# Optimization experiments

Measured on AMD Instinct MI355X. Metric: run time of the kernel, lower is better.

Reference implementation:

```python
import jax, jax.numpy as jnp
import numpy as np

H, DH = 16, 64          # num_heads, dim_head
DIM = 1024              # dim_ltn
EPS = 1e-5


def setup_inputs() -> dict:
    key = jax.random.key(0)
    ks = jax.random.split(key, 8)
    b, n_txt, t, m = 2, 2048, 4, 256
    text = jax.random.normal(ks[0], (b, n_txt, DIM), dtype=jnp.float32)
    image = jax.random.normal(ks[1], (b, t, m, DIM), dtype=jnp.float32)
    locations = jax.random.randint(ks[2], (b, n_txt), 0, 2)  # 0/1 media markers
    s = DIM ** -0.5
    Wq = jax.random.normal(ks[3], (DIM, H * DH), dtype=jnp.float32) * s
    Wkv = jax.random.normal(ks[4], (DIM, 2 * H * DH), dtype=jnp.float32) * s
    Wo = jax.random.normal(ks[5], (H * DH, DIM), dtype=jnp.float32) * s
    ln_gamma = jnp.ones((DIM,), dtype=jnp.float32)
    ln_beta = jnp.zeros((DIM,), dtype=jnp.float32)
    return {"text": text, "image": image, "locations": locations,
            "Wq": Wq, "Wkv": Wkv, "Wo": Wo,
            "ln_gamma": ln_gamma, "ln_beta": ln_beta}


def reference(text, image, locations, Wq, Wkv, Wo, ln_gamma, ln_beta):
    scale = DH ** -0.5
    b, t, m, d = image.shape
    # LayerNorm(text)
    mu = text.mean(-1, keepdims=True)
    var = ((text - mu) ** 2).mean(-1, keepdims=True)
    tn = (text - mu) / jnp.sqrt(var + EPS) * ln_gamma + ln_beta
    img = image.reshape(b, t * m, d)             # b (t m) d
    q = tn @ Wq                                  # b n (h dh)
    k, v = jnp.split(img @ Wkv, 2, axis=-1)      # each b tm (h dh)
    split_heads = lambda x: x.reshape(x.shape[0], x.shape[1], H, DH).transpose(0, 2, 1, 3)
    q, k, v = split_heads(q), split_heads(k), split_heads(v)
    attn = jnp.einsum('bhid,bhjd->bhij', q, k) * scale   # b h n (t m)
    txt_time = jnp.cumsum(locations, axis=-1)            # b n : media index per text token
    viz_time = jnp.repeat(jnp.arange(1, t + 1), m)       # (t m)
    # only_attend_to_immediate -> equality mask
    mask = txt_time[:, None, :, None] == viz_time[None, None, None, :]
    neg = -jnp.finfo(attn.dtype).max
    attn = jnp.where(mask, attn, neg)
    attn = jax.nn.softmax(attn, axis=-1)
    # zero attention for text tokens before any media (txt_time == 0)
    attn = jnp.where((txt_time == 0)[:, None, :, None], 0.0, attn)
    out = jnp.einsum('bhij,bhjd->bhid', attn, v)
    out = out.transpose(0, 2, 1, 3).reshape(b, -1, H * DH)
    return out @ Wo
```

## Files before the change

kernel.cpp:

```cpp
#include <hip/hip_runtime.h>

#define BATCH 2
#define NTXT  2048
#define TMED  4
#define MMED  256
#define TM    (TMED * MMED)
#define DIM   1024
#define NH    16
#define DHD   64
#define KVW   2048
#define RMAX  256
#define RT    32

typedef _Float16 f16x8 __attribute__((ext_vector_type(8)));
typedef float    f32x4 __attribute__((ext_vector_type(4)));

__global__ __launch_bounds__(1024) void k1_scan_ibar(
    const int* __restrict__ loc, const float* __restrict__ image,
    int* __restrict__ tt, int* __restrict__ seg, float* __restrict__ ibar,
    _Float16* __restrict__ img16) {
  __shared__ int buf[NTXT];
  __shared__ int s_start, s_end;
  const int idx = blockIdx.x;
  const int tid = threadIdx.x;
  if (idx < BATCH) {
    const int b = idx;
    if (tid == 0) { s_start = NTXT; s_end = NTXT; }
    buf[tid]        = loc[b * NTXT + tid];
    buf[tid + 1024] = loc[b * NTXT + tid + 1024];
    __syncthreads();
    for (int off = 1; off < NTXT; off <<= 1) {
      int a0 = (tid >= off) ? buf[tid - off] : 0;
      int a1 = buf[tid + 1024 - off];
      __syncthreads();
      buf[tid] += a0;
      buf[tid + 1024] += a1;
      __syncthreads();
    }
    const int v0 = buf[tid], v1 = buf[tid + 1024];
    tt[b * NTXT + tid]        = v0;
    tt[b * NTXT + tid + 1024] = v1;
    if (v0 >= 1) atomicMin(&s_start, tid);
    if (v0 >= 5) atomicMin(&s_end, tid);
    if (v1 >= 1) atomicMin(&s_start, tid + 1024);
    if (v1 >= 5) atomicMin(&s_end, tid + 1024);
    __syncthreads();
    if (tid == 0) {
      seg[b * 2]     = s_start;
      seg[b * 2 + 1] = s_end - s_start;
    }
  } else {
    const int j = idx - BATCH;
    const int b = j >> 3, rt = j & 7;
    const size_t base = (size_t)(b * TM + rt * 128) * DIM + tid;
    const float* p = image + base;
    _Float16* q = img16 + base;
    float s = 0.f;
#pragma unroll 4
    for (int r = 0; r < 128; r++) {
      const float v = p[(size_t)r * DIM];
      s += v;
      q[(size_t)r * DIM] = (_Float16)v;
    }
    atomicAdd(&ibar[b * DIM + tid], s * (1.0f / (float)TM));
  }
}

__global__ __launch_bounds__(256) void k2_prep(
    const float* __restrict__ Wkv, const float* __restrict__ text,
    const float* __restrict__ gamma, const float* __restrict__ beta,
    const int* __restrict__ seg, const float* __restrict__ ibar,
    _Float16* __restrict__ WkvT, float* __restrict__ tn,
    float* __restrict__ vbar) {
  __shared__ float tile[64][65];
  __shared__ float red[256];
  const int idx = blockIdx.x;
  const int tid = threadIdx.x;
  if (idx < 512) {
    const int k0 = (idx & 15) * 64, n0 = (idx >> 4) * 64;
    const int r = tid >> 4, c4 = (tid & 15) * 4;
#pragma unroll
    for (int i = 0; i < 4; i++) {
      const float4 v = *reinterpret_cast<const float4*>(
          Wkv + (size_t)(k0 + r + i * 16) * KVW + n0 + c4);
      tile[r + i * 16][c4 + 0] = v.x; tile[r + i * 16][c4 + 1] = v.y;
      tile[r + i * 16][c4 + 2] = v.z; tile[r + i * 16][c4 + 3] = v.w;
    }
    __syncthreads();
#pragma unroll
    for (int it = 0; it < 2; it++) {
      const int chunk = it * 256 + tid;
      const int n = chunk >> 3, kc = (chunk & 7) * 8;
      f16x8 h;
#pragma unroll
      for (int j = 0; j < 8; j++) h[j] = (_Float16)tile[kc + j][n];
      *reinterpret_cast<f16x8*>(WkvT + (size_t)(n0 + n) * DIM + k0 + kc) = h;
    }
  } else if (idx < 576) {
    const int j = idx - 512;
    const int b = j >> 5, rt = j & 31;
    const int i0 = seg[b * 2];
    const int cnt = min(seg[b * 2 + 1], RMAX);
    for (int r = rt; r < cnt; r += RT) {
      const float* xrow = text + (size_t)(b * NTXT + i0 + r) * DIM;
      float x[4];
      float s = 0.f;
#pragma unroll
      for (int u = 0; u < 4; u++) { x[u] = xrow[tid + 256 * u]; s += x[u]; }
      red[tid] = s; __syncthreads();
      for (int st = 128; st > 0; st >>= 1) {
        if (tid < st) red[tid] += red[tid + st];
        __syncthreads();
      }
      const float mu = red[0] * (1.0f / DIM); __syncthreads();
      float vs = 0.f;
#pragma unroll
      for (int u = 0; u < 4; u++) { float d = x[u] - mu; vs += d * d; }
      red[tid] = vs; __syncthreads();
      for (int st = 128; st > 0; st >>= 1) {
        if (tid < st) red[tid] += red[tid + st];
        __syncthreads();
      }
      const float rstd = rsqrtf(red[0] * (1.0f / DIM) + 1e-5f); __syncthreads();
      float* trow = tn + (size_t)(b * RMAX + r) * DIM;
#pragma unroll
      for (int u = 0; u < 4; u++) {
        const int c = tid + 256 * u;
        trow[c] = (x[u] - mu) * rstd * gamma[c] + beta[c];
      }
      __syncthreads();
    }
  } else {
    const int j = idx - 576;
    const int b = j >> 5, et = (j >> 3) & 3, cc = j & 7;
    const int e = et * 256 + tid;
    const int c0 = cc * 128;
    if (tid < 128) red[tid] = ibar[b * DIM + c0 + tid];
    __syncthreads();
    float s = 0.f;
    for (int c = 0; c < 128; c++)
      s += red[c] * Wkv[(size_t)(c0 + c) * KVW + DIM + e];
    atomicAdd(&vbar[b * DIM + e], s);
  }
}

__global__ __launch_bounds__(512) void k3_gemm_qproj_obar(
    const _Float16* __restrict__ img16, const _Float16* __restrict__ WkvT,
    const float* __restrict__ Wq, const float* __restrict__ Wo,
    const float* __restrict__ tn, const float* __restrict__ vbar,
    const int* __restrict__ seg, _Float16* __restrict__ kv16,
    float* __restrict__ qbuf, float* __restrict__ obar) {
  __shared__ char smem[16384];
  const int idx = blockIdx.x;
  const int tid = threadIdx.x;
  if (idx < 256) {
    _Float16* As = (_Float16*)smem;
    _Float16* Bs = As + 128 * 32;
    const int lane = tid & 63, wid = tid >> 6;
    const int wm = wid & 3, wn = wid >> 2;
    const int row0 = (idx >> 4) * 128, col0 = (idx & 15) * 128;
    const int srow = tid >> 2, skc = (tid & 3) * 8;
    const int frow = lane & 15, fq = lane >> 4;
    f32x4 acc[2][4] = {};
    for (int k0 = 0; k0 < DIM; k0 += 32) {
      const f16x8 av = *reinterpret_cast<const f16x8*>(
          img16 + (size_t)(row0 + srow) * DIM + k0 + skc);
      const f16x8 bv = *reinterpret_cast<const f16x8*>(
          WkvT + (size_t)(col0 + srow) * DIM + k0 + skc);
      __syncthreads();
      *reinterpret_cast<f16x8*>(As + tid * 8) = av;
      *reinterpret_cast<f16x8*>(Bs + tid * 8) = bv;
      __syncthreads();
      f16x8 af[2], bf[4];
#pragma unroll
      for (int mt = 0; mt < 2; mt++)
        af[mt] = *reinterpret_cast<const f16x8*>(
            As + (wm * 32 + mt * 16 + frow) * 32 + fq * 8);
#pragma unroll
      for (int nt = 0; nt < 4; nt++)
        bf[nt] = *reinterpret_cast<const f16x8*>(
            Bs + (wn * 64 + nt * 16 + frow) * 32 + fq * 8);
#pragma unroll
      for (int mt = 0; mt < 2; mt++)
#pragma unroll
        for (int nt = 0; nt < 4; nt++)
          acc[mt][nt] = __builtin_amdgcn_mfma_f32_16x16x32_f16(
              af[mt], bf[nt], acc[mt][nt], 0, 0, 0);
    }
#pragma unroll
    for (int mt = 0; mt < 2; mt++)
#pragma unroll
      for (int nt = 0; nt < 4; nt++) {
        const int col = col0 + wn * 64 + nt * 16 + frow;
#pragma unroll
        for (int r = 0; r < 4; r++) {
          const int row = row0 + wm * 32 + mt * 16 + fq * 4 + r;
          kv16[(size_t)row * KVW + col] = (_Float16)acc[mt][nt][r];
        }
      }
  } else if (idx < 320) {
    float* tn_s = (float*)smem;
    const int j = idx - 256;
    const int b = j >> 5, nt = (j >> 2) & 7, cc = j & 3;
    const int n0 = nt * 128, c0 = cc * 256;
    const int n = tid & 127, cs = tid >> 7;
    const int cnt = min(seg[b * 2 + 1], RMAX);
    for (int r0 = 0; r0 < cnt; r0 += 8) {
      const int rows = min(8, cnt - r0);
      for (int i = tid; i < 8 * 256; i += 512) {
        const int r = i >> 8, c = i & 255;
        tn_s[i] = (r < rows) ? tn[(size_t)(b * RMAX + r0 + r) * DIM + c0 + c]
                             : 0.f;
      }
      __syncthreads();
      float acc[8] = {};
      for (int ci = 0; ci < 64; ci++) {
        const int c = cs * 64 + ci;
        const float w = Wq[(size_t)(c0 + c) * DIM + n0 + n];
#pragma unroll
        for (int rr = 0; rr < 8; rr++) acc[rr] += tn_s[rr * 256 + c] * w;
      }
      for (int rr = 0; rr < rows; rr++)
        atomicAdd(&qbuf[(size_t)(b * RMAX + r0 + rr) * DIM + n0 + n], acc[rr]);
      __syncthreads();
    }
  } else {
    float* vb_s = (float*)smem;
    const int j = idx - 320;
    const int b = j >> 4, et = (j >> 3) & 1, cc = j & 7;
    const int e = et * 512 + tid;
    const int c0 = cc * 128;
    if (tid < 128) vb_s[tid] = vbar[b * DIM + c0 + tid];
    __syncthreads();
    float s = 0.f;
    for (int c = 0; c < 128; c++)
      s += vb_s[c] * Wo[(size_t)(c0 + c) * DIM + e];
    atomicAdd(&obar[b * DIM + e], s);
  }
}

__global__ __launch_bounds__(256) void k4_fill_attn(
    const float* __restrict__ text, const _Float16* __restrict__ kv16,
    const float* __restrict__ Wq, const float* __restrict__ Wo,
    const float* __restrict__ gamma, const float* __restrict__ beta,
    const int* __restrict__ tt, const int* __restrict__ seg,
    const float* __restrict__ obar, const float* __restrict__ qbuf,
    float* __restrict__ oacc, float* __restrict__ out) {
  __shared__ float red[256];
  __shared__ float pbuf[256];
  const int idx = blockIdx.x;
  const int tid = threadIdx.x;
  if (idx < BATCH * NTXT) {
    const int b = idx >> 11;
    const int i = idx & (NTXT - 1);
    const int t = tt[b * NTXT + i];
    float* orow = out + (size_t)(b * NTXT + i) * DIM;
    if (t == 0) {
      for (int c = tid; c < DIM; c += 256) orow[c] = 0.f;
      return;
    }
    if (t > TMED) {
      const float* ob = obar + b * DIM;
      for (int c = tid; c < DIM; c += 256) orow[c] = ob[c];
      return;
    }
    if (i - seg[b * 2] < RMAX) return;
    __shared__ float tns[DIM];
    __shared__ float qrow[DIM];
    __shared__ float oaccs[DIM];
    const float* xrow = text + (size_t)(b * NTXT + i) * DIM;
    float x[4];
    float s = 0.f;
#pragma unroll
    for (int u = 0; u < 4; u++) { x[u] = xrow[tid + 256 * u]; s += x[u]; }
    red[tid] = s; __syncthreads();
    for (int st = 128; st > 0; st >>= 1) {
      if (tid < st) red[tid] += red[tid + st];
      __syncthreads();
    }
    const float mu = red[0] * (1.0f / DIM); __syncthreads();
    float vs = 0.f;
#pragma unroll
    for (int u = 0; u < 4; u++) { float d = x[u] - mu; vs += d * d; }
    red[tid] = vs; __syncthreads();
    for (int st = 128; st > 0; st >>= 1) {
      if (tid < st) red[tid] += red[tid + st];
      __syncthreads();
    }
    const float rstd = rsqrtf(red[0] * (1.0f / DIM) + 1e-5f); __syncthreads();
#pragma unroll
    for (int u = 0; u < 4; u++) {
      const int c = tid + 256 * u;
      tns[c] = (x[u] - mu) * rstd * gamma[c] + beta[c];
    }
    __syncthreads();
    {
      float qa[4] = {0.f, 0.f, 0.f, 0.f};
      for (int c = 0; c < DIM; c++) {
        const float tv = tns[c];
        const float* w = Wq + (size_t)c * DIM + tid;
#pragma unroll
        for (int u = 0; u < 4; u++) qa[u] += tv * w[256 * u];
      }
#pragma unroll
      for (int u = 0; u < 4; u++) qrow[tid + 256 * u] = qa[u];
    }
    __syncthreads();
    const size_t kvrow0 = (size_t)(b * TM + (t - 1) * MMED) * KVW;
    const int d0 = tid & 63, g = tid >> 6;
    for (int h = 0; h < NH; h++) {
      const _Float16* krow = kv16 + kvrow0 + (size_t)tid * KVW + h * DHD;
      float sc = 0.f;
#pragma unroll
      for (int d = 0; d < DHD; d++) sc += qrow[h * DHD + d] * (float)krow[d];
      sc *= 0.125f;
      red[tid] = sc; __syncthreads();
      for (int st = 128; st > 0; st >>= 1) {
        if (tid < st) red[tid] = fmaxf(red[tid], red[tid + st]);
        __syncthreads();
      }
      const float mx = red[0]; __syncthreads();
      const float e = __expf(sc - mx);
      red[tid] = e; __syncthreads();
      for (int st = 128; st > 0; st >>= 1) {
        if (tid < st) red[tid] += red[tid + st];
        __syncthreads();
      }
      const float inv = 1.0f / red[0]; __syncthreads();
      pbuf[tid] = e * inv; __syncthreads();
      const _Float16* vbase = kv16 + kvrow0 + (size_t)(g * 64) * KVW + DIM + h * DHD + d0;
      float a = 0.f;
#pragma unroll 8
      for (int jj = 0; jj < 64; jj++) a += pbuf[g * 64 + jj] * (float)vbase[(size_t)jj * KVW];
      red[tid] = a; __syncthreads();
      if (tid < 64)
        oaccs[h * DHD + tid] = red[tid] + red[64 + tid] + red[128 + tid] + red[192 + tid];
      __syncthreads();
    }
    float oa[4] = {0.f, 0.f, 0.f, 0.f};
    for (int c = 0; c < DIM; c++) {
      const float ov = oaccs[c];
      const float* w = Wo + (size_t)c * DIM + tid;
#pragma unroll
      for (int u = 0; u < 4; u++) oa[u] += ov * w[256 * u];
    }
#pragma unroll
    for (int u = 0; u < 4; u++) orow[tid + 256 * u] = oa[u];
  } else {
    __shared__ float qs[DHD];
    const int j = idx - BATCH * NTXT;
    const int h = j & 15, rt = (j >> 4) & 31, b = j >> 9;
    const int i0 = seg[b * 2];
    const int cnt = min(seg[b * 2 + 1], RMAX);
    const int d0 = tid & 63, g = tid >> 6;
    for (int r = rt; r < cnt; r += RT) {
      const int i = i0 + r;
      const int t = tt[b * NTXT + i];
      if (tid < 64) qs[tid] = qbuf[(size_t)(b * RMAX + r) * DIM + h * DHD + tid];
      __syncthreads();
      const size_t kvrow0 = (size_t)(b * TM + (t - 1) * MMED) * KVW;
      const _Float16* krow = kv16 + kvrow0 + (size_t)tid * KVW + h * DHD;
      float sc = 0.f;
#pragma unroll
      for (int d = 0; d < DHD; d += 8) {
        const f16x8 kk = *reinterpret_cast<const f16x8*>(krow + d);
#pragma unroll
        for (int u = 0; u < 8; u++) sc += qs[d + u] * (float)kk[u];
      }
      sc *= 0.125f;
      red[tid] = sc; __syncthreads();
      for (int st = 128; st > 0; st >>= 1) {
        if (tid < st) red[tid] = fmaxf(red[tid], red[tid + st]);
        __syncthreads();
      }
      const float mx = red[0]; __syncthreads();
      const float e = __expf(sc - mx);
      red[tid] = e; __syncthreads();
      for (int st = 128; st > 0; st >>= 1) {
        if (tid < st) red[tid] += red[tid + st];
        __syncthreads();
      }
      const float inv = 1.0f / red[0]; __syncthreads();
      pbuf[tid] = e * inv; __syncthreads();
      const _Float16* vbase = kv16 + kvrow0 + (size_t)(g * 64) * KVW + DIM + h * DHD + d0;
      float a = 0.f;
#pragma unroll 8
      for (int jj = 0; jj < 64; jj++) a += pbuf[g * 64 + jj] * (float)vbase[(size_t)jj * KVW];
      red[tid] = a; __syncthreads();
      if (tid < 64)
        oacc[(size_t)(b * RMAX + r) * DIM + h * DHD + tid] =
            red[tid] + red[64 + tid] + red[128 + tid] + red[192 + tid];
      __syncthreads();
    }
  }
}

__global__ __launch_bounds__(256) void k5_oproj(
    const float* __restrict__ oacc, const float* __restrict__ Wo,
    const int* __restrict__ seg, float* __restrict__ out) {
  const int ct = blockIdx.x;
  const int rt = blockIdx.y;
  const int b = blockIdx.z;
  const int i0 = seg[b * 2];
  const int cnt = min(seg[b * 2 + 1], RMAX);
  const int tid = threadIdx.x;
  const int d0 = tid & 63, g = tid >> 6;
  __shared__ float op[4][64];
  for (int r = rt; r < cnt; r += RT) {
    const float* arow = oacc + (size_t)(b * RMAX + r) * DIM;
    const float* wo = Wo + (size_t)(g * 256) * DIM + ct * 64 + d0;
    float s = 0.f;
    for (int c = 0; c < 256; c++) s += arow[g * 256 + c] * wo[(size_t)c * DIM];
    op[g][d0] = s; __syncthreads();
    if (tid < 64)
      out[(size_t)(b * NTXT + i0 + r) * DIM + ct * 64 + tid] =
          op[0][tid] + op[1][tid] + op[2][tid] + op[3][tid];
    __syncthreads();
  }
}

extern "C" void kernel_launch(void* const* d_in, const int* in_sizes, int n_in,
                              void* d_out, int out_size, void* d_ws, size_t ws_size,
                              hipStream_t stream) {
  const float* text  = (const float*)d_in[0];
  const float* image = (const float*)d_in[1];
  const int*   loc   = (const int*)d_in[2];
  const float* Wq    = (const float*)d_in[3];
  const float* Wkv   = (const float*)d_in[4];
  const float* Wo    = (const float*)d_in[5];
  const float* gamma = (const float*)d_in[6];
  const float* beta  = (const float*)d_in[7];
  float* out = (float*)d_out;

  _Float16* kv16  = (_Float16*)d_ws;
  _Float16* WkvT  = kv16 + (size_t)BATCH * TM * KVW;
  float*    oacc  = (float*)WkvT;
  _Float16* img16 = WkvT + (size_t)KVW * DIM;
  float*    tn    = (float*)(img16 + (size_t)BATCH * TM * DIM);
  float*    qbuf  = tn + (size_t)BATCH * RMAX * DIM;
  float*    ibar  = qbuf + (size_t)BATCH * RMAX * DIM;
  float*    vbar  = ibar + BATCH * DIM;
  float*    obar  = vbar + BATCH * DIM;
  int*      tt    = (int*)(obar + BATCH * DIM);
  int*      seg   = tt + BATCH * NTXT;

  hipMemsetAsync(qbuf, 0,
                 ((size_t)BATCH * RMAX * DIM + 3 * BATCH * DIM) * sizeof(float),
                 stream);
  k1_scan_ibar<<<BATCH + 16, 1024, 0, stream>>>(loc, image, tt, seg, ibar, img16);
  k2_prep<<<640, 256, 0, stream>>>(Wkv, text, gamma, beta, seg, ibar,
                                   WkvT, tn, vbar);
  k3_gemm_qproj_obar<<<352, 512, 0, stream>>>(img16, WkvT, Wq, Wo, tn, vbar,
                                              seg, kv16, qbuf, obar);
  k4_fill_attn<<<BATCH * NTXT + NH * RT * BATCH, 256, 0, stream>>>(
      text, kv16, Wq, Wo, gamma, beta, tt, seg, obar, qbuf, oacc, out);
  k5_oproj<<<dim3(16, RT, BATCH), 256, 0, stream>>>(oacc, Wo, seg, out);
}
```

Before: 159.3 us.

## Fuse image fp16 conversion into KV GEMM and replace q atomics with partial buffers

The separate fp32-to-fp16 copy of the image in the scan kernel is removed. The KV GEMM now loads fp32 image rows directly and converts them in registers, which saves a full write and re-read of the half-precision image. The image-mean reduction is spread across 128 blocks instead of 16 to raise parallelism. The Q projection reduces its four column-slice partials in shared memory and writes them to four separate partial buffers, which the attention kernel sums when loading q, so the atomics and the large memset go away. The cost is that the GEMM reads twice as many bytes for its A operand.

```diff
diff --git a/kernel.cpp b/kernel.cpp
--- a/kernel.cpp
+++ b/kernel.cpp
@@ -11,14 +11,14 @@
 #define KVW   2048
 #define RMAX  256
 #define RT    32
+#define QSTR  ((size_t)BATCH * RMAX * DIM)
 
 typedef _Float16 f16x8 __attribute__((ext_vector_type(8)));
 typedef float    f32x4 __attribute__((ext_vector_type(4)));
 
 __global__ __launch_bounds__(1024) void k1_scan_ibar(
     const int* __restrict__ loc, const float* __restrict__ image,
-    int* __restrict__ tt, int* __restrict__ seg, float* __restrict__ ibar,
-    _Float16* __restrict__ img16) {
+    int* __restrict__ tt, int* __restrict__ seg, float* __restrict__ ibar) {
   __shared__ int buf[NTXT];
   __shared__ int s_start, s_end;
   const int idx = blockIdx.x;
@@ -51,17 +51,11 @@
     }
   } else {
     const int j = idx - BATCH;
-    const int b = j >> 3, rt = j & 7;
-    const size_t base = (size_t)(b * TM + rt * 128) * DIM + tid;
-    const float* p = image + base;
-    _Float16* q = img16 + base;
+    const int b = j >> 6, rt = j & 63;
+    const float* p = image + (size_t)(b * TM + rt * 16) * DIM + tid;
     float s = 0.f;
-#pragma unroll 4
-    for (int r = 0; r < 128; r++) {
-      const float v = p[(size_t)r * DIM];
-      s += v;
-      q[(size_t)r * DIM] = (_Float16)v;
-    }
+#pragma unroll
+    for (int r = 0; r < 16; r++) s += p[(size_t)r * DIM];
     atomicAdd(&ibar[b * DIM + tid], s * (1.0f / (float)TM));
   }
 }
@@ -145,12 +139,12 @@
 }
 
 __global__ __launch_bounds__(512) void k3_gemm_qproj_obar(
-    const _Float16* __restrict__ img16, const _Float16* __restrict__ WkvT,
+    const float* __restrict__ image, const _Float16* __restrict__ WkvT,
     const float* __restrict__ Wq, const float* __restrict__ Wo,
     const float* __restrict__ tn, const float* __restrict__ vbar,
     const int* __restrict__ seg, _Float16* __restrict__ kv16,
-    float* __restrict__ qbuf, float* __restrict__ obar) {
-  __shared__ char smem[16384];
+    float* __restrict__ qpart, float* __restrict__ obar) {
+  __shared__ char smem[24576];
   const int idx = blockIdx.x;
   const int tid = threadIdx.x;
   if (idx < 256) {
@@ -163,8 +157,14 @@
     const int frow = lane & 15, fq = lane >> 4;
     f32x4 acc[2][4] = {};
     for (int k0 = 0; k0 < DIM; k0 += 32) {
-      const f16x8 av = *reinterpret_cast<const f16x8*>(
-          img16 + (size_t)(row0 + srow) * DIM + k0 + skc);
+      const float* ap = image + (size_t)(row0 + srow) * DIM + k0 + skc;
+      const float4 a0 = *reinterpret_cast<const float4*>(ap);
+      const float4 a1 = *reinterpret_cast<const float4*>(ap + 4);
+      f16x8 av;
+      av[0] = (_Float16)a0.x; av[1] = (_Float16)a0.y;
+      av[2] = (_Float16)a0.z; av[3] = (_Float16)a0.w;
+      av[4] = (_Float16)a1.x; av[5] = (_Float16)a1.y;
+      av[6] = (_Float16)a1.z; av[7] = (_Float16)a1.w;
       const f16x8 bv = *reinterpret_cast<const f16x8*>(
           WkvT + (size_t)(col0 + srow) * DIM + k0 + skc);
       __syncthreads();
@@ -200,11 +200,13 @@
       }
   } else if (idx < 320) {
     float* tn_s = (float*)smem;
+    float* qred = tn_s + 8 * 256;
     const int j = idx - 256;
     const int b = j >> 5, nt = (j >> 2) & 7, cc = j & 3;
     const int n0 = nt * 128, c0 = cc * 256;
     const int n = tid & 127, cs = tid >> 7;
     const int cnt = min(seg[b * 2 + 1], RMAX);
+    float* qp = qpart + (size_t)cc * QSTR;
     for (int r0 = 0; r0 < cnt; r0 += 8) {
       const int rows = min(8, cnt - r0);
       for (int i = tid; i < 8 * 256; i += 512) {
@@ -220,8 +222,16 @@
 #pragma unroll
         for (int rr = 0; rr < 8; rr++) acc[rr] += tn_s[rr * 256 + c] * w;
       }
-      for (int rr = 0; rr < rows; rr++)
-        atomicAdd(&qbuf[(size_t)(b * RMAX + r0 + rr) * DIM + n0 + n], acc[rr]);
+#pragma unroll
+      for (int rr = 0; rr < 8; rr++) qred[(cs * 8 + rr) * 128 + n] = acc[rr];
+      __syncthreads();
+      if (cs == 0) {
+        for (int rr = 0; rr < rows; rr++) {
+          const float s = qred[rr * 128 + n] + qred[(8 + rr) * 128 + n] +
+                          qred[(16 + rr) * 128 + n] + qred[(24 + rr) * 128 + n];
+          qp[(size_t)(b * RMAX + r0 + rr) * DIM + n0 + n] = s;
+        }
+      }
       __syncthreads();
     }
   } else {
@@ -244,7 +254,7 @@
     const float* __restrict__ Wq, const float* __restrict__ Wo,
     const float* __restrict__ gamma, const float* __restrict__ beta,
     const int* __restrict__ tt, const int* __restrict__ seg,
-    const float* __restrict__ obar, const float* __restrict__ qbuf,
+    const float* __restrict__ obar, const float* __restrict__ qpart,
     float* __restrict__ oacc, float* __restrict__ out) {
   __shared__ float red[256];
   __shared__ float pbuf[256];
@@ -356,7 +366,11 @@
     for (int r = rt; r < cnt; r += RT) {
       const int i = i0 + r;
       const int t = tt[b * NTXT + i];
-      if (tid < 64) qs[tid] = qbuf[(size_t)(b * RMAX + r) * DIM + h * DHD + tid];
+      if (tid < 64) {
+        const size_t qoff = (size_t)(b * RMAX + r) * DIM + h * DHD + tid;
+        qs[tid] = qpart[qoff] + qpart[QSTR + qoff] +
+                  qpart[2 * QSTR + qoff] + qpart[3 * QSTR + qoff];
+      }
       __syncthreads();
       const size_t kvrow0 = (size_t)(b * TM + (t - 1) * MMED) * KVW;
       const _Float16* krow = kv16 + kvrow0 + (size_t)tid * KVW + h * DHD;
@@ -435,24 +449,21 @@
   _Float16* kv16  = (_Float16*)d_ws;
   _Float16* WkvT  = kv16 + (size_t)BATCH * TM * KVW;
   float*    oacc  = (float*)WkvT;
-  _Float16* img16 = WkvT + (size_t)KVW * DIM;
-  float*    tn    = (float*)(img16 + (size_t)BATCH * TM * DIM);
-  float*    qbuf  = tn + (size_t)BATCH * RMAX * DIM;
-  float*    ibar  = qbuf + (size_t)BATCH * RMAX * DIM;
+  float*    tn    = (float*)(WkvT + (size_t)KVW * DIM);
+  float*    qpart = tn + (size_t)BATCH * RMAX * DIM;
+  float*    ibar  = qpart + 4 * QSTR;
   float*    vbar  = ibar + BATCH * DIM;
   float*    obar  = vbar + BATCH * DIM;
   int*      tt    = (int*)(obar + BATCH * DIM);
   int*      seg   = tt + BATCH * NTXT;
 
-  hipMemsetAsync(qbuf, 0,
-                 ((size_t)BATCH * RMAX * DIM + 3 * BATCH * DIM) * sizeof(float),
-                 stream);
-  k1_scan_ibar<<<BATCH + 16, 1024, 0, stream>>>(loc, image, tt, seg, ibar, img16);
+  hipMemsetAsync(ibar, 0, 3 * BATCH * DIM * sizeof(float), stream);
+  k1_scan_ibar<<<BATCH + 128, 1024, 0, stream>>>(loc, image, tt, seg, ibar);
   k2_prep<<<640, 256, 0, stream>>>(Wkv, text, gamma, beta, seg, ibar,
                                    WkvT, tn, vbar);
-  k3_gemm_qproj_obar<<<352, 512, 0, stream>>>(img16, WkvT, Wq, Wo, tn, vbar,
-                                              seg, kv16, qbuf, obar);
+  k3_gemm_qproj_obar<<<352, 512, 0, stream>>>(image, WkvT, Wq, Wo, tn, vbar,
+                                              seg, kv16, qpart, obar);
   k4_fill_attn<<<BATCH * NTXT + NH * RT * BATCH, 256, 0, stream>>>(
-      text, kv16, Wq, Wo, gamma, beta, tt, seg, obar, qbuf, oacc, out);
+      text, kv16, Wq, Wo, gamma, beta, tt, seg, obar, qpart, oacc, out);
   k5_oproj<<<dim3(16, RT, BATCH), 256, 0, stream>>>(oacc, Wo, seg, out);
 }
```

Result: slower. 166.3 us (+4.4%).
